# Kernel tuning notes

Measured on AMD Instinct MI355X. Metric: run time of the kernel, lower is better.

The kernel has to match this reference:

```python
import jax, jax.numpy as jnp
import numpy as np

BN_EPS = 1e-5


def _square_distance(src, dst):
    # src: (B,N,3), dst: (B,S,3) -> (B,N,S) squared euclidean distance
    d = -2.0 * jnp.einsum('bnc,bsc->bns', src, dst)
    d += jnp.sum(src * src, -1)[:, :, None]
    d += jnp.sum(dst * dst, -1)[:, None, :]
    return d


def _bn_relu(x, gamma, beta):
    # training-mode BatchNorm1d over (B, C, N): stats over (B, N)
    mean = jnp.mean(x, axis=(0, 2), keepdims=True)
    var = jnp.var(x, axis=(0, 2), keepdims=True)  # biased, as torch uses for normalization
    xhat = (x - mean) * jax.lax.rsqrt(var + BN_EPS)
    return jax.nn.relu(xhat * gamma[None, :, None] + beta[None, :, None])


def setup_inputs() -> dict:
    key = jax.random.key(0)
    ks = jax.random.split(key, 8)
    B, N, S, C1, C2 = 4, 8192, 2048, 128, 256
    inp = {
        'xyz1': jax.random.normal(ks[0], (B, 3, N), jnp.float32),
        'xyz2': jax.random.normal(ks[1], (B, 3, S), jnp.float32),
        'points1': jax.random.normal(ks[2], (B, C1, N), jnp.float32),
        'points2': jax.random.normal(ks[3], (B, C2, S), jnp.float32),
        'w0': jax.random.normal(ks[4], (256, C1 + C2), jnp.float32) * (1.0 / np.sqrt(C1 + C2)),
        'b0': jnp.zeros((256,), jnp.float32),
        'gamma0': jnp.ones((256,), jnp.float32),
        'beta0': jnp.zeros((256,), jnp.float32),
        'w1': jax.random.normal(ks[5], (128, 256), jnp.float32) * (1.0 / np.sqrt(256)),
        'b1': jnp.zeros((128,), jnp.float32),
        'gamma1': jnp.ones((128,), jnp.float32),
        'beta1': jnp.zeros((128,), jnp.float32),
    }
    return inp


def reference(xyz1, xyz2, points1, points2, w0, b0, gamma0, beta0, w1, b1, gamma1, beta1):
    B, _, N = xyz1.shape
    S = xyz2.shape[2]
    xyz1_t = jnp.transpose(xyz1, (0, 2, 1))  # (B,N,3)
    xyz2_t = jnp.transpose(xyz2, (0, 2, 1))  # (B,S,3)
    dist = _square_distance(xyz1_t, xyz2_t)  # (B,N,S)
    neg_d3, idx = jax.lax.top_k(-dist, 3)    # 3 smallest distances
    d3 = -neg_d3                             # (B,N,3)
    dist_recip = 1.0 / (d3 + 1e-8)
    weight = dist_recip / jnp.sum(dist_recip, axis=2, keepdims=True)  # (B,N,3)
    points2_t = jnp.transpose(points2, (0, 2, 1))  # (B,S,C2)
    bidx = jnp.arange(B)[:, None, None]
    neighbor = points2_t[bidx, idx]                 # (B,N,3,C2)
    interp = jnp.sum(neighbor * weight[..., None], axis=2)  # (B,N,C2)
    interp = jnp.transpose(interp, (0, 2, 1))               # (B,C2,N)
    x = jnp.concatenate([points1, interp], axis=1)          # (B,C1+C2,N)
    x = _bn_relu(jnp.einsum('oc,bcn->bon', w0, x) + b0[None, :, None], gamma0, beta0)
    x = _bn_relu(jnp.einsum('oc,bcn->bon', w1, x) + b1[None, :, None], gamma1, beta1)
    return x
```

## Files before the change

### kernel.cpp

```cpp
#include <hip/hip_runtime.h>
#include <hip/hip_bf16.h>

#define BATCH 4
#define NPTS  8192
#define SPTS  2048
#define C1    128
#define C2    256
#define CIN   384
#define H0    256
#define H1    128
#define NSLICE 32

typedef __attribute__((ext_vector_type(8))) short bf16x8;
typedef __attribute__((ext_vector_type(4))) float f32x4;

__device__ __forceinline__ unsigned short f2bf(float x) {
  union { float f; unsigned u; } v; v.f = x;
  unsigned r = v.u + 0x7fff + ((v.u >> 16) & 1);
  return (unsigned short)(r >> 16);
}
__device__ __forceinline__ float bf2f(unsigned short u) {
  union { unsigned u; float f; } v; v.u = ((unsigned)u) << 16; return v.f;
}

__global__ __launch_bounds__(256) void prep_kernel(
    const float* __restrict__ p2, unsigned short* __restrict__ p2tb,
    const float* __restrict__ xyz2, float4* __restrict__ xp,
    const float* __restrict__ w0, const float* __restrict__ w1,
    unsigned short* __restrict__ Wp,
    const float* __restrict__ p1, unsigned short* __restrict__ Xp,
    float* __restrict__ stats) {
  __shared__ unsigned short shmem[64 * 136];
  int bid = blockIdx.x;
  int t = threadIdx.x;

  if (bid < 512) {
    int b = bid >> 7, rem = bid & 127;
    int s0 = (rem >> 2) * 64, c0 = (rem & 3) * 64;
    const float* src = p2 + (size_t)b * C2 * SPTS;
    int ss = t & 63, cseg = t >> 6;
#pragma unroll
    for (int i = 0; i < 16; i++) {
      int cc = cseg + i * 4;
      shmem[ss * 72 + cc] = f2bf(src[(size_t)(c0 + cc) * SPTS + s0 + ss]);
    }
    __syncthreads();
    int s = t >> 2, chunk = t & 3;
    uint4 v0 = *(const uint4*)&shmem[s * 72 + chunk * 16];
    uint4 v1 = *(const uint4*)&shmem[s * 72 + chunk * 16 + 8];
    unsigned short* dst = p2tb + (size_t)b * SPTS * C2 + (size_t)(s0 + s) * C2 + c0 + chunk * 16;
    *(uint4*)dst = v0;
    *(uint4*)(dst + 8) = v1;
  } else if (bid < 1024) {
    int b2 = bid - 512;
    int b = b2 >> 7, n0 = (b2 & 127) * 64;
    int nn = t & 63, c4 = t >> 6;
#pragma unroll
    for (int i = 0; i < 32; i++) {
      int c = i * 4 + c4;
      shmem[nn * 136 + c] = f2bf(p1[((size_t)b * C1 + c) * NPTS + n0 + nn]);
    }
    __syncthreads();
    int n = t >> 2;
#pragma unroll
    for (int j = 0; j < 4; j++) {
      int ch = (t & 3) + j * 4;
      uint4 v = *(const uint4*)&shmem[n * 136 + ch * 8];
      *(uint4*)&Xp[((size_t)b * NPTS + n0 + n) * CIN + ch * 8] = v;
    }
  } else if (bid < 1056) {
    int idx = (bid - 1024) * 256 + t;
    int b = idx >> 11, s = idx & (SPTS - 1);
    const float* x2 = xyz2 + (size_t)b * 3 * SPTS;
    float x = x2[s], y = x2[SPTS + s], z = x2[2 * SPTS + s];
    xp[idx] = make_float4(x, y, z, x * x + y * y + z * z);
  } else if (bid < 1184) {
    int idx = ((bid - 1056) * 256 + t) * 4;
    const float* src = (idx < H0 * CIN) ? (w0 + idx) : (w1 + (idx - H0 * CIN));
    float4 v = *(const float4*)src;
    ushort4 o;
    o.x = f2bf(v.x); o.y = f2bf(v.y); o.z = f2bf(v.z); o.w = f2bf(v.w);
    *(ushort4*)(Wp + idx) = o;
  } else {
    int i4 = ((bid - 1184) * 256 + t) * 4;
    if (i4 < NSLICE * 768) *(float4*)(stats + i4) = make_float4(0.f, 0.f, 0.f, 0.f);
  }
}

#define INS3(d, s, e0, e1, e2, j0, j1, j2)                        \
  {                                                               \
    bool lt0 = (d) < (e0), lt1 = (d) < (e1), lt2 = (d) < (e2);    \
    j2 = lt1 ? (j1) : (lt2 ? (s) : (j2));                         \
    j1 = lt0 ? (j0) : (lt1 ? (s) : (j1));                         \
    j0 = lt0 ? (s) : (j0);                                        \
    e2 = __builtin_amdgcn_fmed3f((d), (e1), (e2));                \
    e1 = __builtin_amdgcn_fmed3f((d), (e0), (e1));                \
    e0 = fminf((d), (e0));                                        \
  }

__global__ __launch_bounds__(1024) void knn_kernel(
    const float* __restrict__ xyz1, const float4* __restrict__ xp,
    int* __restrict__ nidx, float* __restrict__ nw) {
  int b = blockIdx.y;
  int t = threadIdx.x;
  int lane = t & 63;
  int w = __builtin_amdgcn_readfirstlane(t >> 6);
  int n = blockIdx.x * 64 + lane;
  const float* x1 = xyz1 + (size_t)b * 3 * NPTS;
  float px = x1[n], py = x1[NPTS + n], pz = x1[2 * NPTS + n];

  const int CHUNK = SPTS / 16;
  int sbase = w * CHUNK;
  const float4* cp = xp + (size_t)b * SPTS + sbase;

  float d0 = 3e38f, d1 = 3e38f, d2 = 3e38f;
  int i0 = 0, i1 = 0, i2 = 0;
#pragma unroll 8
  for (int j = 0; j < CHUNK; j++) {
    float4 c = cp[j];
    float qc = fmaf(py, c.y, px * c.x);
    qc = fmaf(pz, c.z, qc);
    float d = fmaf(-2.f, qc, c.w);
    int s = sbase + j;
    INS3(d, s, d0, d1, d2, i0, i1, i2);
  }

  __shared__ float dsh[16][64][3];
  __shared__ int   ish[16][64][3];
  dsh[w][lane][0] = d0; dsh[w][lane][1] = d1; dsh[w][lane][2] = d2;
  ish[w][lane][0] = i0; ish[w][lane][1] = i1; ish[w][lane][2] = i2;
  __syncthreads();

  if (t < 256) {
    int g = t >> 6, q = t & 63;
    float e0 = 3e38f, e1 = 3e38f, e2 = 3e38f;
    int j0 = 0, j1 = 0, j2 = 0;
#pragma unroll
    for (int c = 0; c < 4; c++) {
#pragma unroll
      for (int k = 0; k < 3; k++) {
        float d = dsh[4 * g + c][q][k];
        int s = ish[4 * g + c][q][k];
        INS3(d, s, e0, e1, e2, j0, j1, j2);
      }
    }
    dsh[4 * g][q][0] = e0; dsh[4 * g][q][1] = e1; dsh[4 * g][q][2] = e2;
    ish[4 * g][q][0] = j0; ish[4 * g][q][1] = j1; ish[4 * g][q][2] = j2;
  }
  __syncthreads();

  if (t < 64) {
    float e0 = 3e38f, e1 = 3e38f, e2 = 3e38f;
    int j0 = 0, j1 = 0, j2 = 0;
#pragma unroll
    for (int c = 0; c < 4; c++) {
#pragma unroll
      for (int k = 0; k < 3; k++) {
        float d = dsh[4 * c][t][k];
        int s = ish[4 * c][t][k];
        INS3(d, s, e0, e1, e2, j0, j1, j2);
      }
    }
    float qq = px * px + py * py + pz * pz;
    float r0 = 1.f / (e0 + qq + 1e-8f);
    float r1 = 1.f / (e1 + qq + 1e-8f);
    float r2 = 1.f / (e2 + qq + 1e-8f);
    float rs = 1.f / (r0 + r1 + r2);
    int base = (b * NPTS + n) * 3;
    nidx[base + 0] = j0; nidx[base + 1] = j1; nidx[base + 2] = j2;
    nw[base + 0] = r0 * rs; nw[base + 1] = r1 * rs; nw[base + 2] = r2 * rs;
  }
}

__global__ __launch_bounds__(256) void interp_kernel(
    const unsigned short* __restrict__ p2tb, const int* __restrict__ nidx,
    const float* __restrict__ nw, unsigned short* __restrict__ Xp) {
  const int PTS = 8;
  int bid = blockIdx.x;
  int b = bid / (NPTS / PTS);
  int p0 = (bid % (NPTS / PTS)) * PTS;
  int c = threadIdx.x;
  const unsigned short* base = p2tb + (size_t)b * SPTS * C2;
#pragma unroll
  for (int k = 0; k < PTS; k++) {
    int p = p0 + k;
    int ib = (b * NPTS + p) * 3;
    int i0 = nidx[ib], i1 = nidx[ib + 1], i2 = nidx[ib + 2];
    float w0v = nw[ib], w1v = nw[ib + 1], w2v = nw[ib + 2];
    float v = w0v * bf2f(base[(size_t)i0 * C2 + c]) +
              w1v * bf2f(base[(size_t)i1 * C2 + c]) +
              w2v * bf2f(base[(size_t)i2 * C2 + c]);
    Xp[((size_t)b * NPTS + p) * CIN + C1 + c] = f2bf(v);
  }
}

template <int MT, int KD, bool OUT_BF16>
__global__ __launch_bounds__(256) void mfma_gemm_kernel(
    const unsigned short* __restrict__ A, const unsigned short* __restrict__ X,
    const float* __restrict__ bias, void* __restrict__ Yv,
    float* __restrict__ stats, int sum_off, int sq_off) {
  __shared__ unsigned short As[3][128 * 32];
  __shared__ unsigned short Bs[3][128 * 32];
  int b = blockIdx.z;
  int n0 = blockIdx.x * 128;
  int o0 = blockIdx.y * 128;
  int t = threadIdx.x;
  int lane = t & 63;
  int w = __builtin_amdgcn_readfirstlane(t >> 6);
  int mhalf = (w & 1) * 64, nhalf = (w >> 1) * 64;
  const unsigned short* Xb = X + (size_t)b * NPTS * KD;

  int rA = lane >> 2;
  int cofs = (lane & 3) * 8;

  auto stage = [&](int buf, int k0) {
#pragma unroll
    for (int q = 0; q < 2; q++) {
      int r0 = w * 32 + q * 16;
      const unsigned short* ga = A + (size_t)(o0 + r0 + rA) * KD + k0 + cofs;
      __builtin_amdgcn_global_load_lds(
          (const __attribute__((address_space(1))) void*)ga,
          (__attribute__((address_space(3))) void*)(&As[buf][r0 * 32]), 16, 0, 0);
      const unsigned short* gb = Xb + (size_t)(n0 + r0 + rA) * KD + k0 + cofs;
      __builtin_amdgcn_global_load_lds(
          (const __attribute__((address_space(1))) void*)gb,
          (__attribute__((address_space(3))) void*)(&Bs[buf][r0 * 32]), 16, 0, 0);
    }
  };

  constexpr int NT = KD / 32;
  f32x4 acc[4][4] = {};
  int mi = lane & 15, kq = (lane >> 4) * 8;

  stage(0, 0);
  stage(1, 32);

#pragma unroll
  for (int kt = 0; kt < NT; ++kt) {
    if (kt < NT - 1) asm volatile("s_waitcnt vmcnt(4)" ::: "memory");
    else             asm volatile("s_waitcnt vmcnt(0)" ::: "memory");
    __builtin_amdgcn_s_barrier();
    asm volatile("" ::: "memory");
    __builtin_amdgcn_sched_barrier(0);

    if (kt + 2 < NT) stage((kt + 2) % 3, (kt + 2) * 32);

    const unsigned short* Ac = As[kt % 3];
    const unsigned short* Bc = Bs[kt % 3];
    bf16x8 af[4], bfr[4];
#pragma unroll
    for (int i = 0; i < 4; i++) {
      af[i]  = *(const bf16x8*)(Ac + (mhalf + i * 16 + mi) * 32 + kq);
      bfr[i] = *(const bf16x8*)(Bc + (nhalf + i * 16 + mi) * 32 + kq);
    }
#pragma unroll
    for (int mt = 0; mt < 4; mt++)
#pragma unroll
      for (int nt = 0; nt < 4; nt++)
        acc[mt][nt] = __builtin_amdgcn_mfma_f32_16x16x32_bf16(
            af[mt], bfr[nt], acc[mt][nt], 0, 0, 0);
  }

  int slice = ((blockIdx.x << 2) + blockIdx.z) & (NSLICE - 1);
  float* sb = stats + slice * 768 + sum_off;
  float* qb = stats + slice * 768 + sq_off;

  int rq = (lane >> 4) * 4;
#pragma unroll
  for (int mt = 0; mt < 4; mt++) {
#pragma unroll
    for (int r = 0; r < 4; r++) {
      int m = o0 + mhalf + mt * 16 + rq + r;
      float bv = bias[m];
      float ps = 0.f, pq = 0.f;
#pragma unroll
      for (int nt = 0; nt < 4; nt++) {
        int n = n0 + nhalf + nt * 16 + mi;
        float v = acc[mt][nt][r] + bv;
        ps += v; pq += v * v;
        if constexpr (OUT_BF16) {
          unsigned short* Y = (unsigned short*)Yv + (size_t)b * MT * NPTS;
          Y[(size_t)m * NPTS + n] = f2bf(v);
        } else {
          float* Y = (float*)Yv + (size_t)b * MT * NPTS;
          Y[(size_t)m * NPTS + n] = v;
        }
      }
#pragma unroll
      for (int off = 1; off < 16; off <<= 1) {
        ps += __shfl_xor(ps, off, 16);
        pq += __shfl_xor(pq, off, 16);
      }
      if (mi == 0) {
        atomicAdd(&sb[m], ps);
        atomicAdd(&qb[m], pq);
      }
    }
  }
}

__global__ __launch_bounds__(256) void bn0_apply_kernel(
    const unsigned short* __restrict__ Y0, const float* __restrict__ stats,
    const float* __restrict__ gamma, const float* __restrict__ beta,
    unsigned short* __restrict__ X1) {
  __shared__ unsigned short tile[64][80];
  __shared__ float aS[64], sS[64];
  int b = blockIdx.z, o0 = blockIdx.y * 64, n0 = blockIdx.x * 64;
  int t = threadIdx.x;
  if (t < 64) {
    float ms = 0.f, vs = 0.f;
#pragma unroll
    for (int sl = 0; sl < NSLICE; sl++) {
      ms += stats[sl * 768 + o0 + t];
      vs += stats[sl * 768 + 256 + o0 + t];
    }
    const float inv = 1.f / (float)(BATCH * NPTS);
    float mean = ms * inv;
    float var = vs * inv - mean * mean;
    float ia = gamma[o0 + t] * rsqrtf(var + 1e-5f);
    aS[t] = ia; sS[t] = beta[o0 + t] - mean * ia;
  }
  __syncthreads();
  int nn = t & 63, o4 = t >> 6;
#pragma unroll
  for (int i = 0; i < 16; i++) {
    int o = i * 4 + o4;
    float v = bf2f(Y0[((size_t)b * H0 + o0 + o) * NPTS + n0 + nn]);
    v = fmaxf(v * aS[o] + sS[o], 0.f);
    tile[nn][o] = f2bf(v);
  }
  __syncthreads();
  int n = t >> 2;
#pragma unroll
  for (int j = 0; j < 2; j++) {
    int ch = (t & 3) + j * 4;
    uint4 v = *(const uint4*)&tile[n][ch * 8];
    *(uint4*)&X1[((size_t)b * NPTS + n0 + n) * H0 + o0 + ch * 8] = v;
  }
}

__global__ __launch_bounds__(256) void bn_apply_kernel(
    float* __restrict__ Y, const float* __restrict__ stats,
    const float* __restrict__ gamma, const float* __restrict__ beta) {
  __shared__ float sh2[2];
  int idx0 = blockIdx.x * 1024;
  int c = (idx0 >> 13) & (H1 - 1);
  int t = threadIdx.x;
  if (t < 32) {
    float ms = stats[t * 768 + 512 + c];
    float vs = stats[t * 768 + 640 + c];
#pragma unroll
    for (int off = 16; off > 0; off >>= 1) {
      ms += __shfl_down(ms, off, 32);
      vs += __shfl_down(vs, off, 32);
    }
    if (t == 0) {
      const float inv = 1.f / (float)(BATCH * NPTS);
      float mean = ms * inv;
      float var = vs * inv - mean * mean;
      float ia = gamma[c] * rsqrtf(var + 1e-5f);
      sh2[0] = ia; sh2[1] = beta[c] - mean * ia;
    }
  }
  __syncthreads();
  float ia = sh2[0], sh = sh2[1];
  int i = idx0 + t * 4;
  float4 v = *(float4*)(Y + i);
  v.x = fmaxf(v.x * ia + sh, 0.f);
  v.y = fmaxf(v.y * ia + sh, 0.f);
  v.z = fmaxf(v.z * ia + sh, 0.f);
  v.w = fmaxf(v.w * ia + sh, 0.f);
  *(float4*)(Y + i) = v;
}

extern "C" void kernel_launch(void* const* d_in, const int* in_sizes, int n_in,
                              void* d_out, int out_size, void* d_ws, size_t ws_size,
                              hipStream_t stream) {
  const float* xyz1    = (const float*)d_in[0];
  const float* xyz2    = (const float*)d_in[1];
  const float* points1 = (const float*)d_in[2];
  const float* points2 = (const float*)d_in[3];
  const float* w0      = (const float*)d_in[4];
  const float* b0      = (const float*)d_in[5];
  const float* gamma0  = (const float*)d_in[6];
  const float* beta0   = (const float*)d_in[7];
  const float* w1      = (const float*)d_in[8];
  const float* b1      = (const float*)d_in[9];
  const float* gamma1  = (const float*)d_in[10];
  const float* beta1   = (const float*)d_in[11];
  float* out = (float*)d_out;

  char* ws = (char*)d_ws;
  unsigned short* p2tb = (unsigned short*)ws;  ws += (size_t)BATCH * SPTS * C2 * 2;
  unsigned short* Xp = (unsigned short*)ws;    ws += (size_t)BATCH * NPTS * CIN * 2;
  unsigned short* Y0 = (unsigned short*)ws;    ws += (size_t)BATCH * H0 * NPTS * 2;
  unsigned short* X1 = (unsigned short*)ws;    ws += (size_t)BATCH * NPTS * H0 * 2;
  unsigned short* Wp = (unsigned short*)ws;    ws += (size_t)(H0 * CIN + H1 * H0) * 2;
  int* nidx = (int*)ws;                        ws += (size_t)BATCH * NPTS * 3 * 4;
  float* nw = (float*)ws;                      ws += (size_t)BATCH * NPTS * 3 * 4;
  float4* xyz2p = (float4*)(((uintptr_t)ws + 15) & ~(uintptr_t)15);
  ws = (char*)xyz2p + (size_t)BATCH * SPTS * 16;
  float* stats = (float*)ws;                   ws += (size_t)NSLICE * 768 * 4;
  (void)ws_size; (void)in_sizes; (void)n_in; (void)out_size;

  prep_kernel<<<dim3(1208), 256, 0, stream>>>(points2, p2tb, xyz2, xyz2p,
                                              w0, w1, Wp, points1, Xp, stats);
  knn_kernel<<<dim3(NPTS / 64, BATCH), 1024, 0, stream>>>(xyz1, xyz2p, nidx, nw);
  interp_kernel<<<dim3(BATCH * NPTS / 8), 256, 0, stream>>>(p2tb, nidx, nw, Xp);

  mfma_gemm_kernel<H0, CIN, true><<<dim3(NPTS / 128, H0 / 128, BATCH), 256, 0, stream>>>(
      Wp, Xp, b0, Y0, stats, 0, 256);
  bn0_apply_kernel<<<dim3(NPTS / 64, H0 / 64, BATCH), 256, 0, stream>>>(
      Y0, stats, gamma0, beta0, X1);
  mfma_gemm_kernel<H1, H0, false><<<dim3(NPTS / 128, H1 / 128, BATCH), 256, 0, stream>>>(
      Wp + H0 * CIN, X1, b1, out, stats, 512, 640);
  bn_apply_kernel<<<dim3(BATCH * H1 * NPTS / 1024), 256, 0, stream>>>(
      out, stats, gamma1, beta1);
}
```

Before: 189.8 us.

## Fuse kNN with interpolation and fold BN0 apply into second GEMM

Merges the kNN search and the feature interpolation into one kernel that keeps neighbor indices and weights in shared memory, so the separate interpolation launch and its global index round trip go away. The first GEMM now writes its output point-major through an LDS transpose. The second GEMM reduces the BN0 statistics itself and applies normalization plus ReLU while staging its B operand, which removes the bn0_apply kernel and the X1 buffer. The xyz2 prep kernel also pre-scales the coordinates by -2 to save a multiply in the distance loop. In exchange the second GEMM gets a register-staged B path with only double buffering and per-block stat reduction.

```diff
diff --git a/kernel.cpp b/kernel.cpp
--- a/kernel.cpp
+++ b/kernel.cpp
@@ -73,7 +73,7 @@
     int b = idx >> 11, s = idx & (SPTS - 1);
     const float* x2 = xyz2 + (size_t)b * 3 * SPTS;
     float x = x2[s], y = x2[SPTS + s], z = x2[2 * SPTS + s];
-    xp[idx] = make_float4(x, y, z, x * x + y * y + z * z);
+    xp[idx] = make_float4(-2.f * x, -2.f * y, -2.f * z, x * x + y * y + z * z);
   } else if (bid < 1184) {
     int idx = ((bid - 1056) * 256 + t) * 4;
     const float* src = (idx < H0 * CIN) ? (w0 + idx) : (w1 + (idx - H0 * CIN));
@@ -98,9 +98,9 @@
     e0 = fminf((d), (e0));                                        \
   }
 
-__global__ __launch_bounds__(1024) void knn_kernel(
+__global__ __launch_bounds__(1024) void knn_interp_kernel(
     const float* __restrict__ xyz1, const float4* __restrict__ xp,
-    int* __restrict__ nidx, float* __restrict__ nw) {
+    const unsigned short* __restrict__ p2tb, unsigned short* __restrict__ Xp) {
   int b = blockIdx.y;
   int t = threadIdx.x;
   int lane = t & 63;
@@ -118,15 +118,15 @@
 #pragma unroll 8
   for (int j = 0; j < CHUNK; j++) {
     float4 c = cp[j];
-    float qc = fmaf(py, c.y, px * c.x);
-    qc = fmaf(pz, c.z, qc);
-    float d = fmaf(-2.f, qc, c.w);
+    float d = fmaf(c.z, pz, fmaf(c.y, py, fmaf(c.x, px, c.w)));
     int s = sbase + j;
     INS3(d, s, d0, d1, d2, i0, i1, i2);
   }
 
   __shared__ float dsh[16][64][3];
   __shared__ int   ish[16][64][3];
+  __shared__ int   widx[64][3];
+  __shared__ float wwgt[64][3];
   dsh[w][lane][0] = d0; dsh[w][lane][1] = d1; dsh[w][lane][2] = d2;
   ish[w][lane][0] = i0; ish[w][lane][1] = i1; ish[w][lane][2] = i2;
   __syncthreads();
@@ -161,46 +161,43 @@
         INS3(d, s, e0, e1, e2, j0, j1, j2);
       }
     }
-    float qq = px * px + py * py + pz * pz;
+    float qq = fmaf(px, px, fmaf(py, py, pz * pz));
     float r0 = 1.f / (e0 + qq + 1e-8f);
     float r1 = 1.f / (e1 + qq + 1e-8f);
     float r2 = 1.f / (e2 + qq + 1e-8f);
     float rs = 1.f / (r0 + r1 + r2);
-    int base = (b * NPTS + n) * 3;
-    nidx[base + 0] = j0; nidx[base + 1] = j1; nidx[base + 2] = j2;
-    nw[base + 0] = r0 * rs; nw[base + 1] = r1 * rs; nw[base + 2] = r2 * rs;
-  }
-}
-
-__global__ __launch_bounds__(256) void interp_kernel(
-    const unsigned short* __restrict__ p2tb, const int* __restrict__ nidx,
-    const float* __restrict__ nw, unsigned short* __restrict__ Xp) {
-  const int PTS = 8;
-  int bid = blockIdx.x;
-  int b = bid / (NPTS / PTS);
-  int p0 = (bid % (NPTS / PTS)) * PTS;
-  int c = threadIdx.x;
+    widx[t][0] = j0; widx[t][1] = j1; widx[t][2] = j2;
+    wwgt[t][0] = r0 * rs; wwgt[t][1] = r1 * rs; wwgt[t][2] = r2 * rs;
+  }
+  __syncthreads();
+
   const unsigned short* base = p2tb + (size_t)b * SPTS * C2;
-#pragma unroll
-  for (int k = 0; k < PTS; k++) {
-    int p = p0 + k;
-    int ib = (b * NPTS + p) * 3;
-    int i0 = nidx[ib], i1 = nidx[ib + 1], i2 = nidx[ib + 2];
-    float w0v = nw[ib], w1v = nw[ib + 1], w2v = nw[ib + 2];
-    float v = w0v * bf2f(base[(size_t)i0 * C2 + c]) +
-              w1v * bf2f(base[(size_t)i1 * C2 + c]) +
-              w2v * bf2f(base[(size_t)i2 * C2 + c]);
-    Xp[((size_t)b * NPTS + p) * CIN + C1 + c] = f2bf(v);
-  }
-}
-
-template <int MT, int KD, bool OUT_BF16>
-__global__ __launch_bounds__(256) void mfma_gemm_kernel(
+  int c2 = (t & 127) * 2;
+  int psub = t >> 7;
+  unsigned short* xrow = Xp + ((size_t)b * NPTS + blockIdx.x * 64) * CIN + C1 + c2;
+#pragma unroll
+  for (int i = 0; i < 8; i++) {
+    int pl = psub + i * 8;
+    int g0 = widx[pl][0], g1 = widx[pl][1], g2 = widx[pl][2];
+    float w0v = wwgt[pl][0], w1v = wwgt[pl][1], w2v = wwgt[pl][2];
+    unsigned a0 = *(const unsigned*)(base + (size_t)g0 * C2 + c2);
+    unsigned a1 = *(const unsigned*)(base + (size_t)g1 * C2 + c2);
+    unsigned a2 = *(const unsigned*)(base + (size_t)g2 * C2 + c2);
+    float v0 = w0v * bf2f((unsigned short)a0) + w1v * bf2f((unsigned short)a1) +
+               w2v * bf2f((unsigned short)a2);
+    float v1 = w0v * bf2f((unsigned short)(a0 >> 16)) + w1v * bf2f((unsigned short)(a1 >> 16)) +
+               w2v * bf2f((unsigned short)(a2 >> 16));
+    unsigned pk = (unsigned)f2bf(v0) | ((unsigned)f2bf(v1) << 16);
+    *(unsigned*)(xrow + (size_t)pl * CIN) = pk;
+  }
+}
+
+__global__ __launch_bounds__(256) void gemm0_kernel(
     const unsigned short* __restrict__ A, const unsigned short* __restrict__ X,
-    const float* __restrict__ bias, void* __restrict__ Yv,
-    float* __restrict__ stats, int sum_off, int sq_off) {
-  __shared__ unsigned short As[3][128 * 32];
-  __shared__ unsigned short Bs[3][128 * 32];
+    const float* __restrict__ bias, unsigned short* __restrict__ Y0,
+    float* __restrict__ stats) {
+  constexpr int KD = CIN;
+  __shared__ unsigned short lds[24576];
   int b = blockIdx.z;
   int n0 = blockIdx.x * 128;
   int o0 = blockIdx.y * 128;
@@ -209,7 +206,6 @@
   int w = __builtin_amdgcn_readfirstlane(t >> 6);
   int mhalf = (w & 1) * 64, nhalf = (w >> 1) * 64;
   const unsigned short* Xb = X + (size_t)b * NPTS * KD;
-
   int rA = lane >> 2;
   int cofs = (lane & 3) * 8;
 
@@ -220,11 +216,11 @@
       const unsigned short* ga = A + (size_t)(o0 + r0 + rA) * KD + k0 + cofs;
       __builtin_amdgcn_global_load_lds(
           (const __attribute__((address_space(1))) void*)ga,
-          (__attribute__((address_space(3))) void*)(&As[buf][r0 * 32]), 16, 0, 0);
+          (__attribute__((address_space(3))) void*)(lds + buf * 4096 + r0 * 32), 16, 0, 0);
       const unsigned short* gb = Xb + (size_t)(n0 + r0 + rA) * KD + k0 + cofs;
       __builtin_amdgcn_global_load_lds(
           (const __attribute__((address_space(1))) void*)gb,
-          (__attribute__((address_space(3))) void*)(&Bs[buf][r0 * 32]), 16, 0, 0);
+          (__attribute__((address_space(3))) void*)(lds + 12288 + buf * 4096 + r0 * 32), 16, 0, 0);
     }
   };
 
@@ -245,8 +241,8 @@
 
     if (kt + 2 < NT) stage((kt + 2) % 3, (kt + 2) * 32);
 
-    const unsigned short* Ac = As[kt % 3];
-    const unsigned short* Bc = Bs[kt % 3];
+    const unsigned short* Ac = lds + (kt % 3) * 4096;
+    const unsigned short* Bc = lds + 12288 + (kt % 3) * 4096;
     bf16x8 af[4], bfr[4];
 #pragma unroll
     for (int i = 0; i < 4; i++) {
@@ -261,16 +257,159 @@
             af[mt], bfr[nt], acc[mt][nt], 0, 0, 0);
   }
 
+  __syncthreads();
+
   int slice = ((blockIdx.x << 2) + blockIdx.z) & (NSLICE - 1);
-  float* sb = stats + slice * 768 + sum_off;
-  float* qb = stats + slice * 768 + sq_off;
+  float* sb = stats + slice * 768;
+  float* qb = stats + slice * 768 + 256;
 
   int rq = (lane >> 4) * 4;
 #pragma unroll
   for (int mt = 0; mt < 4; mt++) {
 #pragma unroll
     for (int r = 0; r < 4; r++) {
-      int m = o0 + mhalf + mt * 16 + rq + r;
+      int ml = mhalf + mt * 16 + rq + r;
+      float bv = bias[o0 + ml];
+      float ps = 0.f, pq = 0.f;
+#pragma unroll
+      for (int nt = 0; nt < 4; nt++) {
+        int nl = nhalf + nt * 16 + mi;
+        float v = acc[mt][nt][r] + bv;
+        ps += v; pq += v * v;
+        lds[nl * 136 + ml] = f2bf(v);
+      }
+#pragma unroll
+      for (int off = 1; off < 16; off <<= 1) {
+        ps += __shfl_xor(ps, off, 16);
+        pq += __shfl_xor(pq, off, 16);
+      }
+      if (mi == 0) {
+        atomicAdd(&sb[o0 + ml], ps);
+        atomicAdd(&qb[o0 + ml], pq);
+      }
+    }
+  }
+  __syncthreads();
+
+  int row = t >> 1, ch0 = (t & 1) * 64;
+  unsigned short* Yr = Y0 + ((size_t)b * NPTS + n0 + row) * H0 + o0 + ch0;
+#pragma unroll
+  for (int j = 0; j < 8; j++) {
+    uint4 v = *(const uint4*)&lds[row * 136 + ch0 + j * 8];
+    *(uint4*)(Yr + j * 8) = v;
+  }
+}
+
+__global__ __launch_bounds__(256) void gemm1_kernel(
+    const unsigned short* __restrict__ A, const unsigned short* __restrict__ Y0,
+    const float* __restrict__ bias, float* __restrict__ out,
+    float* __restrict__ stats, const float* __restrict__ gamma0,
+    const float* __restrict__ beta0) {
+  constexpr int KD = H0;
+  __shared__ unsigned short As[2][4096];
+  __shared__ unsigned short Bs[2][4096];
+  __shared__ float aS[256], sS[256];
+  int b = blockIdx.z;
+  int n0 = blockIdx.x * 128;
+  int t = threadIdx.x;
+  int lane = t & 63;
+  int w = __builtin_amdgcn_readfirstlane(t >> 6);
+  int mhalf = (w & 1) * 64, nhalf = (w >> 1) * 64;
+  int rA = lane >> 2;
+  int cofs = (lane & 3) * 8;
+  const unsigned short* Yb = Y0 + ((size_t)b * NPTS + n0) * KD;
+
+  {
+    float ms = 0.f, vs = 0.f;
+#pragma unroll 8
+    for (int sl = 0; sl < NSLICE; sl++) {
+      ms += stats[sl * 768 + t];
+      vs += stats[sl * 768 + 256 + t];
+    }
+    const float inv = 1.f / (float)(BATCH * NPTS);
+    float mean = ms * inv;
+    float var = vs * inv - mean * mean;
+    float ia = gamma0[t] * rsqrtf(var + 1e-5f);
+    aS[t] = ia; sS[t] = beta0[t] - mean * ia;
+  }
+  __syncthreads();
+
+  auto stageA = [&](int buf, int k0) {
+#pragma unroll
+    for (int q = 0; q < 2; q++) {
+      int r0 = w * 32 + q * 16;
+      const unsigned short* ga = A + (size_t)(r0 + rA) * KD + k0 + cofs;
+      __builtin_amdgcn_global_load_lds(
+          (const __attribute__((address_space(1))) void*)ga,
+          (__attribute__((address_space(3))) void*)(&As[buf][r0 * 32]), 16, 0, 0);
+    }
+  };
+  bf16x8 br[2];
+  auto loadB = [&](int k0) {
+#pragma unroll
+    for (int q = 0; q < 2; q++) {
+      int r0 = w * 32 + q * 16;
+      br[q] = *(const bf16x8*)(Yb + (size_t)(r0 + rA) * KD + k0 + cofs);
+    }
+  };
+  auto writeB = [&](int buf, int k0) {
+#pragma unroll
+    for (int q = 0; q < 2; q++) {
+      int r0 = w * 32 + q * 16;
+      bf16x8 v = br[q], o;
+#pragma unroll
+      for (int e = 0; e < 8; e++) {
+        float f = bf2f((unsigned short)v[e]);
+        f = fmaxf(fmaf(f, aS[k0 + cofs + e], sS[k0 + cofs + e]), 0.f);
+        o[e] = (short)f2bf(f);
+      }
+      *(bf16x8*)(&Bs[buf][(r0 + rA) * 32 + cofs]) = o;
+    }
+  };
+
+  constexpr int NT = KD / 32;
+  f32x4 acc[4][4] = {};
+  int mi = lane & 15, kq = (lane >> 4) * 8;
+
+  stageA(0, 0);
+  loadB(0);
+  int buf = 0;
+#pragma unroll
+  for (int kt = 0; kt < NT; ++kt) {
+    asm volatile("s_waitcnt vmcnt(0)" ::: "memory");
+    __builtin_amdgcn_sched_barrier(0);
+    writeB(buf, kt * 32);
+    asm volatile("s_waitcnt lgkmcnt(0)" ::: "memory");
+    asm volatile("s_barrier" ::: "memory");
+    __builtin_amdgcn_sched_barrier(0);
+    if (kt + 1 < NT) { stageA(buf ^ 1, (kt + 1) * 32); loadB((kt + 1) * 32); }
+
+    bf16x8 af[4], bfr[4];
+#pragma unroll
+    for (int i = 0; i < 4; i++) {
+      af[i]  = *(const bf16x8*)(&As[buf][(mhalf + i * 16 + mi) * 32 + kq]);
+      bfr[i] = *(const bf16x8*)(&Bs[buf][(nhalf + i * 16 + mi) * 32 + kq]);
+    }
+#pragma unroll
+    for (int mt = 0; mt < 4; mt++)
+#pragma unroll
+      for (int nt = 0; nt < 4; nt++)
+        acc[mt][nt] = __builtin_amdgcn_mfma_f32_16x16x32_bf16(
+            af[mt], bfr[nt], acc[mt][nt], 0, 0, 0);
+    buf ^= 1;
+  }
+
+  int slice = ((blockIdx.x << 2) + blockIdx.z) & (NSLICE - 1);
+  float* sb = stats + slice * 768 + 512;
+  float* qb = stats + slice * 768 + 640;
+  float* Yo = out + (size_t)b * H1 * NPTS;
+
+  int rq = (lane >> 4) * 4;
+#pragma unroll
+  for (int mt = 0; mt < 4; mt++) {
+#pragma unroll
+    for (int r = 0; r < 4; r++) {
+      int m = mhalf + mt * 16 + rq + r;
       float bv = bias[m];
       float ps = 0.f, pq = 0.f;
 #pragma unroll
@@ -278,13 +417,7 @@
         int n = n0 + nhalf + nt * 16 + mi;
         float v = acc[mt][nt][r] + bv;
         ps += v; pq += v * v;
-        if constexpr (OUT_BF16) {
-          unsigned short* Y = (unsigned short*)Yv + (size_t)b * MT * NPTS;
-          Y[(size_t)m * NPTS + n] = f2bf(v);
-        } else {
-          float* Y = (float*)Yv + (size_t)b * MT * NPTS;
-          Y[(size_t)m * NPTS + n] = v;
-        }
+        Yo[(size_t)m * NPTS + n] = v;
       }
 #pragma unroll
       for (int off = 1; off < 16; off <<= 1) {
@@ -296,46 +429,6 @@
         atomicAdd(&qb[m], pq);
       }
     }
-  }
-}
-
-__global__ __launch_bounds__(256) void bn0_apply_kernel(
-    const unsigned short* __restrict__ Y0, const float* __restrict__ stats,
-    const float* __restrict__ gamma, const float* __restrict__ beta,
-    unsigned short* __restrict__ X1) {
-  __shared__ unsigned short tile[64][80];
-  __shared__ float aS[64], sS[64];
-  int b = blockIdx.z, o0 = blockIdx.y * 64, n0 = blockIdx.x * 64;
-  int t = threadIdx.x;
-  if (t < 64) {
-    float ms = 0.f, vs = 0.f;
-#pragma unroll
-    for (int sl = 0; sl < NSLICE; sl++) {
-      ms += stats[sl * 768 + o0 + t];
-      vs += stats[sl * 768 + 256 + o0 + t];
-    }
-    const float inv = 1.f / (float)(BATCH * NPTS);
-    float mean = ms * inv;
-    float var = vs * inv - mean * mean;
-    float ia = gamma[o0 + t] * rsqrtf(var + 1e-5f);
-    aS[t] = ia; sS[t] = beta[o0 + t] - mean * ia;
-  }
-  __syncthreads();
-  int nn = t & 63, o4 = t >> 6;
-#pragma unroll
-  for (int i = 0; i < 16; i++) {
-    int o = i * 4 + o4;
-    float v = bf2f(Y0[((size_t)b * H0 + o0 + o) * NPTS + n0 + nn]);
-    v = fmaxf(v * aS[o] + sS[o], 0.f);
-    tile[nn][o] = f2bf(v);
-  }
-  __syncthreads();
-  int n = t >> 2;
-#pragma unroll
-  for (int j = 0; j < 2; j++) {
-    int ch = (t & 3) + j * 4;
-    uint4 v = *(const uint4*)&tile[n][ch * 8];
-    *(uint4*)&X1[((size_t)b * NPTS + n0 + n) * H0 + o0 + ch * 8] = v;
   }
 }
 
@@ -393,11 +486,8 @@
   char* ws = (char*)d_ws;
   unsigned short* p2tb = (unsigned short*)ws;  ws += (size_t)BATCH * SPTS * C2 * 2;
   unsigned short* Xp = (unsigned short*)ws;    ws += (size_t)BATCH * NPTS * CIN * 2;
-  unsigned short* Y0 = (unsigned short*)ws;    ws += (size_t)BATCH * H0 * NPTS * 2;
-  unsigned short* X1 = (unsigned short*)ws;    ws += (size_t)BATCH * NPTS * H0 * 2;
+  unsigned short* Y0 = (unsigned short*)ws;    ws += (size_t)BATCH * NPTS * H0 * 2;
   unsigned short* Wp = (unsigned short*)ws;    ws += (size_t)(H0 * CIN + H1 * H0) * 2;
-  int* nidx = (int*)ws;                        ws += (size_t)BATCH * NPTS * 3 * 4;
-  float* nw = (float*)ws;                      ws += (size_t)BATCH * NPTS * 3 * 4;
   float4* xyz2p = (float4*)(((uintptr_t)ws + 15) & ~(uintptr_t)15);
   ws = (char*)xyz2p + (size_t)BATCH * SPTS * 16;
   float* stats = (float*)ws;                   ws += (size_t)NSLICE * 768 * 4;
@@ -405,15 +495,11 @@
 
   prep_kernel<<<dim3(1208), 256, 0, stream>>>(points2, p2tb, xyz2, xyz2p,
                                               w0, w1, Wp, points1, Xp, stats);
-  knn_kernel<<<dim3(NPTS / 64, BATCH), 1024, 0, stream>>>(xyz1, xyz2p, nidx, nw);
-  interp_kernel<<<dim3(BATCH * NPTS / 8), 256, 0, stream>>>(p2tb, nidx, nw, Xp);
-
-  mfma_gemm_kernel<H0, CIN, true><<<dim3(NPTS / 128, H0 / 128, BATCH), 256, 0, stream>>>(
-      Wp, Xp, b0, Y0, stats, 0, 256);
-  bn0_apply_kernel<<<dim3(NPTS / 64, H0 / 64, BATCH), 256, 0, stream>>>(
-      Y0, stats, gamma0, beta0, X1);
-  mfma_gemm_kernel<H1, H0, false><<<dim3(NPTS / 128, H1 / 128, BATCH), 256, 0, stream>>>(
-      Wp + H0 * CIN, X1, b1, out, stats, 512, 640);
+  knn_interp_kernel<<<dim3(NPTS / 64, BATCH), 1024, 0, stream>>>(xyz1, xyz2p, p2tb, Xp);
+  gemm0_kernel<<<dim3(NPTS / 128, H0 / 128, BATCH), 256, 0, stream>>>(
+      Wp, Xp, b0, Y0, stats);
+  gemm1_kernel<<<dim3(NPTS / 128, 1, BATCH), 256, 0, stream>>>(
+      Wp + H0 * CIN, Y0, b1, out, stats, gamma0, beta0);
   bn_apply_kernel<<<dim3(BATCH * H1 * NPTS / 1024), 256, 0, stream>>>(
       out, stats, gamma1, beta1);
 }
```

New measurement: 180.8 us. 4.7% less time.
